# Kernel optimization log

Hardware: AMD Instinct MI355X
Metric: run time of the kernel (lower is better)

## Reference

```python
import jax, jax.numpy as jnp
import numpy as np

V, E, U, B, T = 128, 256, 1024, 32, 256


def setup_inputs() -> dict:
    key = jax.random.key(0)
    ks = iter(jax.random.split(key, 64))
    def p(shape, scale=0.05):
        return jax.random.normal(next(ks), shape, jnp.float32) * scale
    inp = {
        "x": jax.random.randint(next(ks), (B, T), 0, V),
        "emb": p((V, E), 1.0),
        "fc_W": p((2 * U, V)),
        "fc_b": jnp.zeros((V,), jnp.float32),
    }
    for l in range(3):
        din = E if l == 0 else 2 * U
        for d in ("fw", "bw"):
            inp[f"Wg_{d}{l}"] = p((din + U, 2 * U))   # fused r,u gate kernel
            inp[f"bg_{d}{l}"] = jnp.ones((2 * U,), jnp.float32)  # TF GRUCell ones bias init
            inp[f"Wc_{d}{l}"] = p((din + U, U))       # candidate kernel
            inp[f"bc_{d}{l}"] = jnp.zeros((U,), jnp.float32)
            inp[f"h_{d}{l}"] = jnp.zeros((B, U), jnp.float32)
    return inp


def _gru_scan(x_seq, h0, Wg, bg, Wc, bc, reverse):
    # x_seq: [T, B, din]; TF contrib GRUCell math.
    def step(h, xt):
        ru = jax.nn.sigmoid(jnp.concatenate([xt, h], -1) @ Wg + bg)
        r, u = jnp.split(ru, 2, axis=-1)
        c = jnp.tanh(jnp.concatenate([xt, r * h], -1) @ Wc + bc)
        h_new = u * h + (1.0 - u) * c
        return h_new, h_new
    hT, ys = jax.lax.scan(step, h0, x_seq, reverse=reverse)
    return hT, ys  # ys in original time order even when reverse=True


def reference(x, emb, fc_W, fc_b,
              Wg_fw0, bg_fw0, Wc_fw0, bc_fw0, h_fw0,
              Wg_bw0, bg_bw0, Wc_bw0, bc_bw0, h_bw0,
              Wg_fw1, bg_fw1, Wc_fw1, bc_fw1, h_fw1,
              Wg_bw1, bg_bw1, Wc_bw1, bc_bw1, h_bw1,
              Wg_fw2, bg_fw2, Wc_fw2, bc_fw2, h_fw2,
              Wg_bw2, bg_bw2, Wc_bw2, bc_bw2, h_bw2):
    fw = [(Wg_fw0, bg_fw0, Wc_fw0, bc_fw0, h_fw0),
          (Wg_fw1, bg_fw1, Wc_fw1, bc_fw1, h_fw1),
          (Wg_fw2, bg_fw2, Wc_fw2, bc_fw2, h_fw2)]
    bw = [(Wg_bw0, bg_bw0, Wc_bw0, bc_bw0, h_bw0),
          (Wg_bw1, bg_bw1, Wc_bw1, bc_bw1, h_bw1),
          (Wg_bw2, bg_bw2, Wc_bw2, bc_bw2, h_bw2)]
    seq = emb[x].transpose(1, 0, 2)  # [T, B, E]
    states_fw, states_bw = [], []
    for l in range(3):
        Wg, bg, Wc, bc, h0 = fw[l]
        hf, yf = _gru_scan(seq, h0, Wg, bg, Wc, bc, reverse=False)
        Wg, bg, Wc, bc, h0 = bw[l]
        hb, yb = _gru_scan(seq, h0, Wg, bg, Wc, bc, reverse=True)
        seq = jnp.concatenate([yf, yb], axis=-1)  # [T, B, 2U]
        states_fw.append(hf)
        states_bw.append(hb)
    out = seq.transpose(1, 0, 2).reshape(-1, 2 * U)  # [B*T, 2U], batch-major like dynamic_rnn
    logits = out @ fc_W + fc_b
    return (logits, jnp.stack(states_fw), jnp.stack(states_bw))
```

## Files before the change

kernel.cpp:

```cpp
#include <hip/hip_runtime.h>

typedef _Float16 f16;
typedef _Float16 f16x4 __attribute__((ext_vector_type(4)));
typedef _Float16 f16x8 __attribute__((ext_vector_type(8)));
typedef float f32x4 __attribute__((ext_vector_type(4)));

#define NB 32
#define NT 256
#define NE 256
#define NU 1024
#define NV 128

#define MEMF() asm volatile("" ::: "memory")

__device__ __forceinline__ unsigned long long cload64(const f16* p) {
    return __hip_atomic_load((const unsigned long long*)p, __ATOMIC_RELAXED,
                             __HIP_MEMORY_SCOPE_AGENT);
}
__device__ __forceinline__ float cloadf(const float* p) {
    return __hip_atomic_load(p, __ATOMIC_RELAXED, __HIP_MEMORY_SCOPE_AGENT);
}
__device__ __forceinline__ void cstoref(float* p, float v) {
    __hip_atomic_store(p, v, __ATOMIC_RELAXED, __HIP_MEMORY_SCOPE_AGENT);
}
__device__ __forceinline__ void cstore16(f16* p, f16 v) {
    __hip_atomic_store((unsigned short*)p, __builtin_bit_cast(unsigned short, v),
                       __ATOMIC_RELAXED, __HIP_MEMORY_SCOPE_AGENT);
}

__device__ __forceinline__ void barsync() {
    MEMF();
    __builtin_amdgcn_s_barrier();
    MEMF();
}

__device__ __forceinline__ void gwait(const unsigned* flagd, unsigned target) {
    if (threadIdx.x < 64) {
        int it = 0;
        for (;;) {
            unsigned v = __hip_atomic_load(&flagd[threadIdx.x * 16],
                                           __ATOMIC_RELAXED, __HIP_MEMORY_SCOPE_AGENT);
            if (__all(v >= target)) break;
            if (++it > (1 << 16)) break;
        }
    }
}

__device__ __forceinline__ void gbar(unsigned* flagd, int lb, unsigned target) {
    asm volatile("s_waitcnt vmcnt(0)" ::: "memory");
    barsync();
    if (threadIdx.x == 0)
        __hip_atomic_store(&flagd[lb * 16], target, __ATOMIC_RELAXED,
                           __HIP_MEMORY_SCOPE_AGENT);
    gwait(flagd, target);
    barsync();
}

__device__ __forceinline__ void stage32(const f16* __restrict__ src,
                                        f16* __restrict__ stg, int tid) {
    unsigned long long a[16], b[16];
    #pragma unroll
    for (int i = 0; i < 16; ++i)
        a[i] = cload64(src + i * NU + tid * 4);
    MEMF();
    #pragma unroll
    for (int i = 0; i < 16; ++i)
        b[i] = cload64(src + (16 + i) * NU + tid * 4);
    MEMF();
    #pragma unroll
    for (int i = 0; i < 16; ++i)
        *(f16x4*)(&stg[i * 1032 + tid * 4]) = __builtin_bit_cast(f16x4, a[i]);
    #pragma unroll
    for (int i = 0; i < 16; ++i)
        *(f16x4*)(&stg[(16 + i) * 1032 + tid * 4]) = __builtin_bit_cast(f16x4, b[i]);
}

__global__ void embed_kernel(const int* __restrict__ x, const float* __restrict__ emb,
                             f16* __restrict__ seq0) {
    int row = blockIdx.x;
    int t = row >> 5, b = row & 31;
    int e = threadIdx.x;
    int idx = x[b * NT + t];
    seq0[row * NE + e] = (f16)emb[idx * NE + e];
}

__global__ void wconv(const float* __restrict__ Wg, const float* __restrict__ Wc,
                      f16* __restrict__ WgT, f16* __restrict__ WcT, int K2) {
    __shared__ float tile[32][33];
    int mat = blockIdx.z & 1;
    const float* in = mat ? Wc : Wg;
    f16* outp = mat ? WcT : WgT;
    int N = mat ? 1024 : 2048;
    int by = blockIdx.y;
    if (by * 32 >= N) return;
    int k0 = blockIdx.x * 32, n0 = by * 32;
    int tx = threadIdx.x & 31, ty = threadIdx.x >> 5;
    #pragma unroll
    for (int i = 0; i < 4; ++i) {
        int r = ty * 4 + i;
        tile[r][tx] = in[(size_t)(k0 + r) * N + n0 + tx];
    }
    __syncthreads();
    #pragma unroll
    for (int i = 0; i < 4; ++i) {
        int rn = ty * 4 + i;
        outp[(size_t)(n0 + rn) * K2 + k0 + tx] = (f16)tile[tx][rn];
    }
}

__launch_bounds__(256)
__global__ void gemm_projT(const f16* __restrict__ A, int lda, int K,
                           const f16* __restrict__ WgT, const f16* __restrict__ WcT, int K2,
                           const float* __restrict__ bg, const float* __restrict__ bc,
                           f16* __restrict__ proj) {
    __shared__ f16 As[128][40];
    __shared__ f16 Bs[128][40];
    int cb = blockIdx.y;
    const f16* Bsrc; int outcol; const float* bias;
    if (cb < 16) { Bsrc = WgT + (size_t)cb * 128 * K2; outcol = cb * 128; bias = bg + cb * 128; }
    else { Bsrc = WcT + (size_t)(cb - 16) * 128 * K2; outcol = 2048 + (cb - 16) * 128; bias = bc + (cb - 16) * 128; }
    int m0 = blockIdx.x * 128;
    int tid = threadIdx.x;
    int w = tid >> 6, l = tid & 63;
    int wm = w & 1, wn = w >> 1;
    f32x4 acc[4][4] = {};
    for (int k0 = 0; k0 < K; k0 += 32) {
        __syncthreads();
        #pragma unroll
        for (int p = 0; p < 2; ++p) {
            int e = (p * 256 + tid) * 8;
            int r = e >> 5, kq = e & 31;
            f16x8 v = *(const f16x8*)(A + (size_t)(m0 + r) * lda + k0 + kq);
            *(f16x8*)(&As[r][kq]) = v;
        }
        #pragma unroll
        for (int p = 0; p < 2; ++p) {
            int e = (p * 256 + tid) * 8;
            int r = e >> 5, kq = e & 31;
            f16x8 v = *(const f16x8*)(Bsrc + (size_t)r * K2 + k0 + kq);
            *(f16x8*)(&Bs[r][kq]) = v;
        }
        __syncthreads();
        int kq = (l >> 4) * 8;
        f16x8 a[4], b[4];
        #pragma unroll
        for (int i = 0; i < 4; ++i) a[i] = *(const f16x8*)(&As[wm * 64 + i * 16 + (l & 15)][kq]);
        #pragma unroll
        for (int j = 0; j < 4; ++j) b[j] = *(const f16x8*)(&Bs[wn * 64 + j * 16 + (l & 15)][kq]);
        #pragma unroll
        for (int i = 0; i < 4; ++i)
            #pragma unroll
            for (int j = 0; j < 4; ++j)
                acc[i][j] = __builtin_amdgcn_mfma_f32_16x16x32_f16(a[i], b[j], acc[i][j], 0, 0, 0);
    }
    int lr = (l >> 4) * 4, lc = l & 15;
    #pragma unroll
    for (int i = 0; i < 4; ++i) {
        #pragma unroll
        for (int j = 0; j < 4; ++j) {
            int gcol = wn * 64 + j * 16 + lc;
            float bia = bias[gcol];
            #pragma unroll
            for (int q = 0; q < 4; ++q) {
                int grow = m0 + wm * 64 + i * 16 + lr + q;
                proj[(size_t)grow * 3072 + outcol + gcol] = (f16)(acc[i][j][q] + bia);
            }
        }
    }
}

__launch_bounds__(256)
__global__ void gemm_proj(const f16* __restrict__ A, int lda, int K,
                          const float* __restrict__ Wg, const float* __restrict__ Wc,
                          const float* __restrict__ bg, const float* __restrict__ bc,
                          f16* __restrict__ proj) {
    __shared__ f16 As[128][40];
    __shared__ f16 Bs[128][40];
    int cb = blockIdx.y;
    const float* Bsrc; int ldb, outcol; const float* bias;
    if (cb < 16) { Bsrc = Wg + cb * 128; ldb = 2 * NU; outcol = cb * 128; bias = bg + cb * 128; }
    else { Bsrc = Wc + (cb - 16) * 128; ldb = NU; outcol = 2 * NU + (cb - 16) * 128; bias = bc + (cb - 16) * 128; }
    int m0 = blockIdx.x * 128;
    int tid = threadIdx.x;
    int w = tid >> 6, l = tid & 63;
    int wm = w & 1, wn = w >> 1;
    f32x4 acc[4][4] = {};
    for (int k0 = 0; k0 < K; k0 += 32) {
        __syncthreads();
        #pragma unroll
        for (int p = 0; p < 2; ++p) {
            int e = (p * 256 + tid) * 8;
            int r = e >> 5, kq = e & 31;
            f16x8 v = *(const f16x8*)(A + (size_t)(m0 + r) * lda + k0 + kq);
            *(f16x8*)(&As[r][kq]) = v;
        }
        #pragma unroll
        for (int p = 0; p < 4; ++p) {
            int k = p * 8 + (tid >> 5);
            int n = (tid & 31) * 4;
            float4 v = *(const float4*)(Bsrc + (size_t)(k0 + k) * ldb + n);
            Bs[n + 0][k] = (f16)v.x; Bs[n + 1][k] = (f16)v.y;
            Bs[n + 2][k] = (f16)v.z; Bs[n + 3][k] = (f16)v.w;
        }
        __syncthreads();
        int kq = (l >> 4) * 8;
        f16x8 a[4], b[4];
        #pragma unroll
        for (int i = 0; i < 4; ++i) a[i] = *(const f16x8*)(&As[wm * 64 + i * 16 + (l & 15)][kq]);
        #pragma unroll
        for (int j = 0; j < 4; ++j) b[j] = *(const f16x8*)(&Bs[wn * 64 + j * 16 + (l & 15)][kq]);
        #pragma unroll
        for (int i = 0; i < 4; ++i)
            #pragma unroll
            for (int j = 0; j < 4; ++j)
                acc[i][j] = __builtin_amdgcn_mfma_f32_16x16x32_f16(a[i], b[j], acc[i][j], 0, 0, 0);
    }
    int lr = (l >> 4) * 4, lc = l & 15;
    #pragma unroll
    for (int i = 0; i < 4; ++i) {
        #pragma unroll
        for (int j = 0; j < 4; ++j) {
            int gcol = wn * 64 + j * 16 + lc;
            float bia = bias[gcol];
            #pragma unroll
            for (int q = 0; q < 4; ++q) {
                int grow = m0 + wm * 64 + i * 16 + lr + q;
                proj[(size_t)grow * 3072 + outcol + gcol] = (f16)(acc[i][j][q] + bia);
            }
        }
    }
}

__launch_bounds__(256)
__global__ void gemm_fc(const f16* __restrict__ y, const float* __restrict__ W,
                        const float* __restrict__ bias, float* __restrict__ out) {
    __shared__ f16 As[128][40];
    __shared__ f16 Bs[128][40];
    int m0 = blockIdx.x * 128;
    int tid = threadIdx.x;
    int w = tid >> 6, l = tid & 63;
    int wm = w & 1, wn = w >> 1;
    f32x4 acc[4][4] = {};
    for (int k0 = 0; k0 < 2048; k0 += 32) {
        __syncthreads();
        #pragma unroll
        for (int p = 0; p < 2; ++p) {
            int e = (p * 256 + tid) * 8;
            int r = e >> 5, kq = e & 31;
            int grow = m0 + r;
            int b = grow >> 8, t = grow & 255;
            f16x8 v = *(const f16x8*)(y + (size_t)(t * 32 + b) * 2048 + k0 + kq);
            *(f16x8*)(&As[r][kq]) = v;
        }
        #pragma unroll
        for (int p = 0; p < 4; ++p) {
            int k = p * 8 + (tid >> 5);
            int n = (tid & 31) * 4;
            float4 v = *(const float4*)(W + (size_t)(k0 + k) * 128 + n);
            Bs[n + 0][k] = (f16)v.x; Bs[n + 1][k] = (f16)v.y;
            Bs[n + 2][k] = (f16)v.z; Bs[n + 3][k] = (f16)v.w;
        }
        __syncthreads();
        int kq = (l >> 4) * 8;
        f16x8 a[4], b[4];
        #pragma unroll
        for (int i = 0; i < 4; ++i) a[i] = *(const f16x8*)(&As[wm * 64 + i * 16 + (l & 15)][kq]);
        #pragma unroll
        for (int j = 0; j < 4; ++j) b[j] = *(const f16x8*)(&Bs[wn * 64 + j * 16 + (l & 15)][kq]);
        #pragma unroll
        for (int i = 0; i < 4; ++i)
            #pragma unroll
            for (int j = 0; j < 4; ++j)
                acc[i][j] = __builtin_amdgcn_mfma_f32_16x16x32_f16(a[i], b[j], acc[i][j], 0, 0, 0);
    }
    int lr = (l >> 4) * 4, lc = l & 15;
    #pragma unroll
    for (int i = 0; i < 4; ++i) {
        #pragma unroll
        for (int j = 0; j < 4; ++j) {
            int gcol = wn * 64 + j * 16 + lc;
            float bia = bias[gcol];
            #pragma unroll
            for (int q = 0; q < 4; ++q) {
                int grow = m0 + wm * 64 + i * 16 + lr + q;
                out[(size_t)grow * 128 + gcol] = acc[i][j][q] + bia;
            }
        }
    }
}

__launch_bounds__(256)
__global__ void gru_layer(
    const f16* __restrict__ proj_fw, const f16* __restrict__ proj_bw,
    const float* __restrict__ Wgh_fw, const float* __restrict__ Wgh_bw,
    const float* __restrict__ Wch_fw, const float* __restrict__ Wch_bw,
    const float* __restrict__ h0_fw, const float* __restrict__ h0_bw,
    f16* __restrict__ h16, f16* __restrict__ rh16, float* __restrict__ u32,
    f16* __restrict__ y, float* __restrict__ st_fw, float* __restrict__ st_bw,
    unsigned* __restrict__ cnt)
{
    extern __shared__ f16 smem[];
    f16* stg    = smem;
    f16* Wc_lds = smem + 32 * 1032;

    int bid = blockIdx.x, tid = threadIdx.x;
    int dir = bid >> 6, lb = bid & 63;
    int gcb = lb * 32;
    int ccb = lb * 16;

    const f16*  proj = dir ? proj_bw : proj_fw;
    const float* Wgh = dir ? Wgh_bw : Wgh_fw;
    const float* Wch = dir ? Wch_bw : Wch_fw;
    const float* h0  = dir ? h0_bw  : h0_fw;
    f16*   h16d  = h16  + dir * (NB * NU);
    f16*   rh16d = rh16 + dir * (NB * NU);
    float* u32d  = u32  + dir * (NB * NU);
    unsigned* flagd = cnt + dir * 1024;

    int w = tid >> 6, l = tid & 63;
    int lc = l & 15, lr = (l >> 4) * 4, kq = (l >> 4) * 8;
    int wm = w & 1, wn = w >> 1, wb = w & 1;

    {
        int j2 = tid & 15;
        for (int k = tid >> 4; k < NU; k += 16)
            Wc_lds[j2 * 1032 + k] = (f16)Wch[(size_t)k * 1024 + ccb + j2];
    }

    f16x8 wgf[32];
    {
        int col = gcb + wn * 16 + lc;
        #pragma unroll
        for (int kt = 0; kt < 32; ++kt) {
            f16x8 t;
            #pragma unroll
            for (int e = 0; e < 8; ++e)
                t[e] = (f16)Wgh[(size_t)(kt * 32 + kq + e) * 2048 + col];
            wgf[kt] = t;
        }
    }

    {
        int base = lb * 512;
        for (int i = tid; i < 512; i += 256)
            cstore16(h16d + base + i, (f16)h0[base + i]);
    }
    f32x4 hreg = {};
    if (w < 2) {
        #pragma unroll
        for (int q = 0; q < 4; ++q)
            hreg[q] = h0[(size_t)(wb * 16 + lr + q) * NU + ccb + lc];
    }

    int gc  = gcb + wn * 16 + lc;
    int cc  = ccb + lc;
    int cc2 = 2048 + ccb + lc;

    f16 pg[4], pc[4];
    {
        int td0 = dir ? (NT - 1) : 0;
        const f16* pr = proj + (size_t)td0 * NB * 3072;
        #pragma unroll
        for (int q = 0; q < 4; ++q) {
            pg[q] = pr[(size_t)(wm * 16 + lr + q) * 3072 + gc];
            pc[q] = pr[(size_t)(wb * 16 + lr + q) * 3072 + cc2];
        }
    }

    unsigned bc = 1;
    gbar(flagd, lb, bc);

    for (int tl = 0; tl < NT; ++tl) {
        int td = dir ? (NT - 1 - tl) : tl;

        stage32(h16d, stg, tid);
        asm volatile("s_waitcnt lgkmcnt(0)" ::: "memory");
        __builtin_amdgcn_sched_barrier(0);
        barsync();

        {
            const f16* ap = &stg[(wm * 16 + lc) * 1032 + kq];
            f32x4 acc0 = {}, acc1 = {};
            #pragma unroll
            for (int kt = 0; kt < 32; kt += 2) {
                f16x8 a0 = *(const f16x8*)(ap + kt * 32);
                f16x8 a1 = *(const f16x8*)(ap + (kt + 1) * 32);
                acc0 = __builtin_amdgcn_mfma_f32_16x16x32_f16(a0, wgf[kt], acc0, 0, 0, 0);
                acc1 = __builtin_amdgcn_mfma_f32_16x16x32_f16(a1, wgf[kt + 1], acc1, 0, 0, 0);
            }
            f32x4 acc = acc0 + acc1;
            #pragma unroll
            for (int q = 0; q < 4; ++q) {
                int br = wm * 16 + lr + q;
                float pre = acc[q] + (float)pg[q];
                float sg = 1.f / (1.f + __expf(-pre));
                if (gc < NU) {
                    float hv = (float)stg[br * 1032 + gc];
                    cstore16(rh16d + br * NU + gc, (f16)(sg * hv));
                } else {
                    cstoref(u32d + br * NU + gc - NU, sg);
                }
            }
        }
        ++bc;
        gbar(flagd, lb, bc);

        float uu[4];
        if (w < 2) {
            #pragma unroll
            for (int q = 0; q < 4; ++q)
                uu[q] = cloadf(u32d + (wb * 16 + lr + q) * NU + cc);
        }

        stage32(rh16d, stg, tid);
        asm volatile("s_waitcnt lgkmcnt(0)" ::: "memory");
        __builtin_amdgcn_sched_barrier(0);
        barsync();

        if (w < 2) {
            const f16* ap = &stg[(wb * 16 + lc) * 1032 + kq];
            const f16* bptr = Wc_lds + lc * 1032 + kq;
            f32x4 acc0 = {}, acc1 = {};
            #pragma unroll
            for (int kt = 0; kt < 32; kt += 2) {
                f16x8 a0 = *(const f16x8*)(ap + kt * 32);
                f16x8 a1 = *(const f16x8*)(ap + (kt + 1) * 32);
                f16x8 b0 = *(const f16x8*)(bptr + kt * 32);
                f16x8 b1 = *(const f16x8*)(bptr + kt * 32 + 32);
                acc0 = __builtin_amdgcn_mfma_f32_16x16x32_f16(a0, b0, acc0, 0, 0, 0);
                acc1 = __builtin_amdgcn_mfma_f32_16x16x32_f16(a1, b1, acc1, 0, 0, 0);
            }
            f32x4 acc = acc0 + acc1;
            #pragma unroll
            for (int q = 0; q < 4; ++q) {
                int br = wb * 16 + lr + q;
                float pre = acc[q] + (float)pc[q];
                float e2 = __expf(2.f * pre);
                float c = 1.f - 2.f / (e2 + 1.f);
                float hn = uu[q] * hreg[q] + (1.f - uu[q]) * c;
                hreg[q] = hn;
                cstore16(h16d + br * NU + cc, (f16)hn);
            }
        }
        ++bc;
        asm volatile("s_waitcnt vmcnt(0)" ::: "memory");
        barsync();
        if (tid == 0)
            __hip_atomic_store(&flagd[lb * 16], bc, __ATOMIC_RELAXED,
                               __HIP_MEMORY_SCOPE_AGENT);
        if (w < 2) {
            #pragma unroll
            for (int q = 0; q < 4; ++q) {
                int br = wb * 16 + lr + q;
                y[(size_t)(td * NB + br) * 2048 + dir * NU + cc] = (f16)hreg[q];
                if (tl == NT - 1)
                    (dir ? st_bw : st_fw)[br * NU + cc] = hreg[q];
            }
        }
        if (tl + 1 < NT) {
            int tdn = dir ? (NT - 2 - tl) : (tl + 1);
            const f16* pr = proj + (size_t)tdn * NB * 3072;
            #pragma unroll
            for (int q = 0; q < 4; ++q) {
                pg[q] = pr[(size_t)(wm * 16 + lr + q) * 3072 + gc];
                pc[q] = pr[(size_t)(wb * 16 + lr + q) * 3072 + cc2];
            }
        }
        gwait(flagd, bc);
        barsync();
    }
}

extern "C" void kernel_launch(void* const* d_in, const int* in_sizes, int n_in,
                              void* d_out, int out_size, void* d_ws, size_t ws_size,
                              hipStream_t stream) {
    const int*   x   = (const int*)  d_in[0];
    const float* emb = (const float*)d_in[1];
    const float* fcW = (const float*)d_in[2];
    const float* fcb = (const float*)d_in[3];
    float* out = (float*)d_out;

    char* ws = (char*)d_ws;
    size_t off = 0;
    f16* seq0   = (f16*)(ws + off); off += (size_t)8192 * 256 * 2;
    f16* ybuf0  = (f16*)(ws + off); off += (size_t)8192 * 2048 * 2;
    f16* ybuf1  = (f16*)(ws + off); off += (size_t)8192 * 2048 * 2;
    f16* projfw = (f16*)(ws + off); off += (size_t)8192 * 3072 * 2;
    f16* projbw = (f16*)(ws + off); off += (size_t)8192 * 3072 * 2;
    f16*   h16  = (f16*)(ws + off);   off += 2 * 32 * 1024 * 2;
    f16*   rh16 = (f16*)(ws + off);   off += 2 * 32 * 1024 * 2;
    float* u32  = (float*)(ws + off); off += 2 * 32 * 1024 * 4;
    unsigned* ctrl = (unsigned*)(ws + off); off += 3 * 8192;
    f16* WgT_fw = (f16*)(ws + off); off += (size_t)2048 * 3072 * 2;
    f16* WgT_bw = (f16*)(ws + off); off += (size_t)2048 * 3072 * 2;
    f16* WcT_fw = (f16*)(ws + off); off += (size_t)1024 * 3072 * 2;
    f16* WcT_bw = (f16*)(ws + off); off += (size_t)1024 * 3072 * 2;
    bool cvt = (ws_size >= off);

    hipFuncSetAttribute((const void*)gru_layer,
                        hipFuncAttributeMaxDynamicSharedMemorySize, 99072);

    hipMemsetAsync(ctrl, 0, 3 * 8192, stream);
    embed_kernel<<<dim3(8192), dim3(256), 0, stream>>>(x, emb, seq0);

    const f16* lin = seq0; int lda = 256, K = 256;
    f16* ybufs[2] = {ybuf0, ybuf1};
    for (int l = 0; l < 3; ++l) {
        const float* Wg_fw = (const float*)d_in[4 + l * 10 + 0];
        const float* bg_fw = (const float*)d_in[4 + l * 10 + 1];
        const float* Wc_fw = (const float*)d_in[4 + l * 10 + 2];
        const float* bc_fw = (const float*)d_in[4 + l * 10 + 3];
        const float* h0_fw = (const float*)d_in[4 + l * 10 + 4];
        const float* Wg_bw = (const float*)d_in[4 + l * 10 + 5];
        const float* bg_bw = (const float*)d_in[4 + l * 10 + 6];
        const float* Wc_bw = (const float*)d_in[4 + l * 10 + 7];
        const float* bc_bw = (const float*)d_in[4 + l * 10 + 8];
        const float* h0_bw = (const float*)d_in[4 + l * 10 + 9];
        int din = (l == 0) ? 256 : 2048;
        int K2 = din + 1024;

        if (cvt) {
            wconv<<<dim3(K2 / 32, 64, 2), dim3(256), 0, stream>>>(Wg_fw, Wc_fw, WgT_fw, WcT_fw, K2);
            wconv<<<dim3(K2 / 32, 64, 2), dim3(256), 0, stream>>>(Wg_bw, Wc_bw, WgT_bw, WcT_bw, K2);
            gemm_projT<<<dim3(64, 24), dim3(256), 0, stream>>>(lin, lda, K, WgT_fw, WcT_fw, K2, bg_fw, bc_fw, projfw);
            gemm_projT<<<dim3(64, 24), dim3(256), 0, stream>>>(lin, lda, K, WgT_bw, WcT_bw, K2, bg_bw, bc_bw, projbw);
        } else {
            gemm_proj<<<dim3(64, 24), dim3(256), 0, stream>>>(lin, lda, K, Wg_fw, Wc_fw, bg_fw, bc_fw, projfw);
            gemm_proj<<<dim3(64, 24), dim3(256), 0, stream>>>(lin, lda, K, Wg_bw, Wc_bw, bg_bw, bc_bw, projbw);
        }

        const float* Wgh_fw = Wg_fw + (size_t)din * 2048;
        const float* Wgh_bw = Wg_bw + (size_t)din * 2048;
        const float* Wch_fw = Wc_fw + (size_t)din * 1024;
        const float* Wch_bw = Wc_bw + (size_t)din * 1024;
        f16* yout = ybufs[l & 1];
        float* stfw = out + 1048576 + l * 32768;
        float* stbw = out + 1048576 + 98304 + l * 32768;
        unsigned* cnt = ctrl + l * 2048;

        gru_layer<<<dim3(128), dim3(256), 99072, stream>>>(
            projfw, projbw, Wgh_fw, Wgh_bw, Wch_fw, Wch_bw, h0_fw, h0_bw,
            h16, rh16, u32, yout, stfw, stbw, cnt);
        lin = yout; lda = 2048; K = 2048;
    }

    gemm_fc<<<dim3(64), dim3(256), 0, stream>>>(ybufs[0], fcW, fcb, out);
}
```

Measured before the change: 6.463 ms.

## Split GRU recurrence by batch halves with independent per-half grid barriers

Each direction's 64 blocks are now partitioned into two independent groups, one per 16-row batch half, and each block owns twice as many gate and candidate columns. Every block stages only its 16 batch rows of h and r*h per step instead of all 32, and each barrier syncs 32 blocks rather than 64. The aim is to halve the global-to-LDS staging traffic per step and shorten the grid-barrier fan-in. The trade-off is that all four waves now do gate MFMAs and each block holds a wider slice of weights, which raises per-block work, and the flag array doubles in size.

```diff
diff --git a/kernel.cpp b/kernel.cpp
--- a/kernel.cpp
+++ b/kernel.cpp
@@ -38,7 +38,7 @@
     if (threadIdx.x < 64) {
         int it = 0;
         for (;;) {
-            unsigned v = __hip_atomic_load(&flagd[threadIdx.x * 16],
+            unsigned v = __hip_atomic_load(&flagd[(threadIdx.x & 31) * 16],
                                            __ATOMIC_RELAXED, __HIP_MEMORY_SCOPE_AGENT);
             if (__all(v >= target)) break;
             if (++it > (1 << 16)) break;
@@ -46,33 +46,26 @@
     }
 }
 
-__device__ __forceinline__ void gbar(unsigned* flagd, int lb, unsigned target) {
+__device__ __forceinline__ void gbar(unsigned* flagd, int cg, unsigned target) {
     asm volatile("s_waitcnt vmcnt(0)" ::: "memory");
     barsync();
     if (threadIdx.x == 0)
-        __hip_atomic_store(&flagd[lb * 16], target, __ATOMIC_RELAXED,
+        __hip_atomic_store(&flagd[cg * 16], target, __ATOMIC_RELAXED,
                            __HIP_MEMORY_SCOPE_AGENT);
     gwait(flagd, target);
     barsync();
 }
 
-__device__ __forceinline__ void stage32(const f16* __restrict__ src,
+__device__ __forceinline__ void stage16(const f16* __restrict__ src,
                                         f16* __restrict__ stg, int tid) {
-    unsigned long long a[16], b[16];
+    unsigned long long a[16];
     #pragma unroll
     for (int i = 0; i < 16; ++i)
         a[i] = cload64(src + i * NU + tid * 4);
     MEMF();
     #pragma unroll
     for (int i = 0; i < 16; ++i)
-        b[i] = cload64(src + (16 + i) * NU + tid * 4);
-    MEMF();
-    #pragma unroll
-    for (int i = 0; i < 16; ++i)
         *(f16x4*)(&stg[i * 1032 + tid * 4]) = __builtin_bit_cast(f16x4, a[i]);
-    #pragma unroll
-    for (int i = 0; i < 16; ++i)
-        *(f16x4*)(&stg[(16 + i) * 1032 + tid * 4]) = __builtin_bit_cast(f16x4, b[i]);
 }
 
 __global__ void embed_kernel(const int* __restrict__ x, const float* __restrict__ emb,
@@ -301,12 +294,15 @@
 {
     extern __shared__ f16 smem[];
     f16* stg    = smem;
-    f16* Wc_lds = smem + 32 * 1032;
+    f16* Wc_lds = smem + 16 * 1032;
 
     int bid = blockIdx.x, tid = threadIdx.x;
     int dir = bid >> 6, lb = bid & 63;
-    int gcb = lb * 32;
-    int ccb = lb * 16;
+    int rh_i = lb >> 5;
+    int cg   = lb & 31;
+    int R0   = rh_i * 16;
+    int gcb  = cg * 64;
+    int ccb  = cg * 32;
 
     const f16*  proj = dir ? proj_bw : proj_fw;
     const float* Wgh = dir ? Wgh_bw : Wgh_fw;
@@ -315,21 +311,23 @@
     f16*   h16d  = h16  + dir * (NB * NU);
     f16*   rh16d = rh16 + dir * (NB * NU);
     float* u32d  = u32  + dir * (NB * NU);
-    unsigned* flagd = cnt + dir * 1024;
+    unsigned* flagd = cnt + (dir * 2 + rh_i) * 1024;
+
+    const f16* hsrc  = h16d  + (size_t)R0 * NU;
+    const f16* rhsrc = rh16d + (size_t)R0 * NU;
 
     int w = tid >> 6, l = tid & 63;
     int lc = l & 15, lr = (l >> 4) * 4, kq = (l >> 4) * 8;
-    int wm = w & 1, wn = w >> 1, wb = w & 1;
 
     {
-        int j2 = tid & 15;
-        for (int k = tid >> 4; k < NU; k += 16)
+        int j2 = tid & 31;
+        for (int k = tid >> 5; k < NU; k += 8)
             Wc_lds[j2 * 1032 + k] = (f16)Wch[(size_t)k * 1024 + ccb + j2];
     }
 
     f16x8 wgf[32];
     {
-        int col = gcb + wn * 16 + lc;
+        int col = gcb + w * 16 + lc;
         #pragma unroll
         for (int kt = 0; kt < 32; ++kt) {
             f16x8 t;
@@ -349,12 +347,13 @@
     if (w < 2) {
         #pragma unroll
         for (int q = 0; q < 4; ++q)
-            hreg[q] = h0[(size_t)(wb * 16 + lr + q) * NU + ccb + lc];
-    }
-
-    int gc  = gcb + wn * 16 + lc;
-    int cc  = ccb + lc;
-    int cc2 = 2048 + ccb + lc;
+            hreg[q] = h0[(size_t)(R0 + lr + q) * NU + ccb + w * 16 + lc];
+    }
+
+    int gc  = gcb + w * 16 + lc;
+    int cc  = ccb + (w & 1) * 16 + lc;
+    int cc2 = 2048 + cc;
+    bool rblk = (cg < 16);
 
     f16 pg[4], pc[4];
     {
@@ -362,24 +361,24 @@
         const f16* pr = proj + (size_t)td0 * NB * 3072;
         #pragma unroll
         for (int q = 0; q < 4; ++q) {
-            pg[q] = pr[(size_t)(wm * 16 + lr + q) * 3072 + gc];
-            pc[q] = pr[(size_t)(wb * 16 + lr + q) * 3072 + cc2];
+            pg[q] = pr[(size_t)(R0 + lr + q) * 3072 + gc];
+            pc[q] = pr[(size_t)(R0 + lr + q) * 3072 + cc2];
         }
     }
 
     unsigned bc = 1;
-    gbar(flagd, lb, bc);
+    gbar(flagd, cg, bc);
 
     for (int tl = 0; tl < NT; ++tl) {
         int td = dir ? (NT - 1 - tl) : tl;
 
-        stage32(h16d, stg, tid);
+        stage16(hsrc, stg, tid);
         asm volatile("s_waitcnt lgkmcnt(0)" ::: "memory");
         __builtin_amdgcn_sched_barrier(0);
         barsync();
 
         {
-            const f16* ap = &stg[(wm * 16 + lc) * 1032 + kq];
+            const f16* ap = &stg[lc * 1032 + kq];
             f32x4 acc0 = {}, acc1 = {};
             #pragma unroll
             for (int kt = 0; kt < 32; kt += 2) {
@@ -391,35 +390,35 @@
             f32x4 acc = acc0 + acc1;
             #pragma unroll
             for (int q = 0; q < 4; ++q) {
-                int br = wm * 16 + lr + q;
+                int br = lr + q;
                 float pre = acc[q] + (float)pg[q];
                 float sg = 1.f / (1.f + __expf(-pre));
-                if (gc < NU) {
+                if (rblk) {
                     float hv = (float)stg[br * 1032 + gc];
-                    cstore16(rh16d + br * NU + gc, (f16)(sg * hv));
+                    cstore16(rh16d + (size_t)(R0 + br) * NU + gc, (f16)(sg * hv));
                 } else {
-                    cstoref(u32d + br * NU + gc - NU, sg);
+                    cstoref(u32d + (size_t)(R0 + br) * NU + gc - NU, sg);
                 }
             }
         }
         ++bc;
-        gbar(flagd, lb, bc);
+        gbar(flagd, cg, bc);
 
         float uu[4];
         if (w < 2) {
             #pragma unroll
             for (int q = 0; q < 4; ++q)
-                uu[q] = cloadf(u32d + (wb * 16 + lr + q) * NU + cc);
-        }
-
-        stage32(rh16d, stg, tid);
+                uu[q] = cloadf(u32d + (size_t)(R0 + lr + q) * NU + cc);
+        }
+
+        stage16(rhsrc, stg, tid);
         asm volatile("s_waitcnt lgkmcnt(0)" ::: "memory");
         __builtin_amdgcn_sched_barrier(0);
         barsync();
 
         if (w < 2) {
-            const f16* ap = &stg[(wb * 16 + lc) * 1032 + kq];
-            const f16* bptr = Wc_lds + lc * 1032 + kq;
+            const f16* ap = &stg[lc * 1032 + kq];
+            const f16* bptr = Wc_lds + ((w & 1) * 16 + lc) * 1032 + kq;
             f32x4 acc0 = {}, acc1 = {};
             #pragma unroll
             for (int kt = 0; kt < 32; kt += 2) {
@@ -433,28 +432,28 @@
             f32x4 acc = acc0 + acc1;
             #pragma unroll
             for (int q = 0; q < 4; ++q) {
-                int br = wb * 16 + lr + q;
+                int br = R0 + lr + q;
                 float pre = acc[q] + (float)pc[q];
                 float e2 = __expf(2.f * pre);
                 float c = 1.f - 2.f / (e2 + 1.f);
                 float hn = uu[q] * hreg[q] + (1.f - uu[q]) * c;
                 hreg[q] = hn;
-                cstore16(h16d + br * NU + cc, (f16)hn);
+                cstore16(h16d + (size_t)br * NU + cc, (f16)hn);
             }
         }
         ++bc;
         asm volatile("s_waitcnt vmcnt(0)" ::: "memory");
         barsync();
         if (tid == 0)
-            __hip_atomic_store(&flagd[lb * 16], bc, __ATOMIC_RELAXED,
+            __hip_atomic_store(&flagd[cg * 16], bc, __ATOMIC_RELAXED,
                                __HIP_MEMORY_SCOPE_AGENT);
         if (w < 2) {
             #pragma unroll
             for (int q = 0; q < 4; ++q) {
-                int br = wb * 16 + lr + q;
+                int br = R0 + lr + q;
                 y[(size_t)(td * NB + br) * 2048 + dir * NU + cc] = (f16)hreg[q];
                 if (tl == NT - 1)
-                    (dir ? st_bw : st_fw)[br * NU + cc] = hreg[q];
+                    (dir ? st_bw : st_fw)[(size_t)br * NU + cc] = hreg[q];
             }
         }
         if (tl + 1 < NT) {
@@ -462,8 +461,8 @@
             const f16* pr = proj + (size_t)tdn * NB * 3072;
             #pragma unroll
             for (int q = 0; q < 4; ++q) {
-                pg[q] = pr[(size_t)(wm * 16 + lr + q) * 3072 + gc];
-                pc[q] = pr[(size_t)(wb * 16 + lr + q) * 3072 + cc2];
+                pg[q] = pr[(size_t)(R0 + lr + q) * 3072 + gc];
+                pc[q] = pr[(size_t)(R0 + lr + q) * 3072 + cc2];
             }
         }
         gwait(flagd, bc);
@@ -490,7 +489,7 @@
     f16*   h16  = (f16*)(ws + off);   off += 2 * 32 * 1024 * 2;
     f16*   rh16 = (f16*)(ws + off);   off += 2 * 32 * 1024 * 2;
     float* u32  = (float*)(ws + off); off += 2 * 32 * 1024 * 4;
-    unsigned* ctrl = (unsigned*)(ws + off); off += 3 * 8192;
+    unsigned* ctrl = (unsigned*)(ws + off); off += 3 * 16384;
     f16* WgT_fw = (f16*)(ws + off); off += (size_t)2048 * 3072 * 2;
     f16* WgT_bw = (f16*)(ws + off); off += (size_t)2048 * 3072 * 2;
     f16* WcT_fw = (f16*)(ws + off); off += (size_t)1024 * 3072 * 2;
@@ -500,7 +499,7 @@
     hipFuncSetAttribute((const void*)gru_layer,
                         hipFuncAttributeMaxDynamicSharedMemorySize, 99072);
 
-    hipMemsetAsync(ctrl, 0, 3 * 8192, stream);
+    hipMemsetAsync(ctrl, 0, 3 * 16384, stream);
     embed_kernel<<<dim3(8192), dim3(256), 0, stream>>>(x, emb, seq0);
 
     const f16* lin = seq0; int lda = 256, K = 256;
@@ -536,7 +535,7 @@
         f16* yout = ybufs[l & 1];
         float* stfw = out + 1048576 + l * 32768;
         float* stbw = out + 1048576 + 98304 + l * 32768;
-        unsigned* cnt = ctrl + l * 2048;
+        unsigned* cnt = ctrl + l * 4096;
 
         gru_layer<<<dim3(128), dim3(256), 99072, stream>>>(
             projfw, projbw, Wgh_fw, Wgh_bw, Wch_fw, Wch_bw, h0_fw, h0_bw,
```

New measurement: 5.765 ms. -10.8%, faster.
